# Optimization experiments

Hardware: AMD Instinct MI355X
Metric: run time of the kernel (lower is better)

## Reference

```python
import jax, jax.numpy as jnp
import numpy as np


def _dnn(a, b):
    # tf.math.divide_no_nan
    safe = jnp.where(b == 0, 1.0, b)
    return jnp.where(b == 0, 0.0, a / safe)


def _safe_sqrt(x):
    # _sqrt: 0 where x == 0 (grad-safe)
    p = x > 0
    return jnp.where(p, jnp.sqrt(jnp.where(p, x, 1.0)), 0.0)


def _agg4(v):
    # mean/var/skew/kurt over last axis, using the sample skew/kurt formulas
    # from _skewness2/_kurtosis2 in the source.
    n = float(v.shape[-1])
    m = jnp.mean(v, -1)
    c = v - m[..., None]
    var = jnp.mean(c ** 2, -1)
    std = _safe_sqrt(var)
    skew = n / ((n - 1.0) * (n - 2.0)) * jnp.sum(_dnn(c, std[..., None]) ** 3, -1)
    k4 = jnp.sum(c ** 4, -1)
    k22 = jnp.sum(c ** 2, -1) ** 2
    alpha = n * (n + 1.0) * (n - 1.0) / (n - 2.0) / (n - 3.0)
    kurt = alpha * _dnn(k4, k22) - 3.0 * (n - 1.0) ** 2 / (n - 2.0) / (n - 3.0)
    return m, var, skew, kurt


def _forward(x):
    B, T, F = x.shape
    nT = float(T)

    mean = jnp.mean(x, 1)                        # [B,F]
    xc = x - mean[:, None, :]                    # x_sub_means
    var = jnp.mean(xc ** 2, 1)                   # population variance
    std = _safe_sqrt(var)
    # diff: conv kernel [0,1,-1] VALID -> d[t] = x[t+1] - x[t+2], len T-2
    xd = x[:, 1:-1, :] - x[:, 2:, :]
    xd_abs = jnp.abs(xd)

    scal = [mean,
            jnp.min(x, 1), jnp.max(x, 1),
            _safe_sqrt(jnp.mean(x ** 2, 1)),      # rms
            var, std]
    # skewness / kurtosis over time (exact formulas from source)
    skew = nT / ((nT - 1.0) * (nT - 2.0)) * jnp.sum(_dnn(xc, std[:, None, :]) ** 3, 1)
    k4 = jnp.sum(xc ** 4, 1)
    k22 = jnp.sum(xc ** 2, 1) ** 2
    alpha = nT * (nT + 1.0) * (nT - 1.0) / (nT - 2.0) / (nT - 3.0)
    kurt = alpha * _dnn(k4, k22) - 3.0 * (nT - 1.0) ** 2 / (nT - 2.0) / (nT - 3.0)
    scal += [skew, kurt,
             jnp.mean(xd, 1), jnp.sum(xd, 1), jnp.mean(xd_abs, 1),  # change stats
             jnp.sum(x ** 2, 1),                  # abs_energy
             jnp.max(jnp.abs(x), 1),              # abs_max
             jnp.sum(xd_abs, 1),                  # abs_sum_of_changes
             _safe_sqrt(jnp.sum(xd ** 2, 1))]     # cid_ce

    # quantiles (sorted) and time-based quantiles
    xs = jnp.sort(x, axis=1)
    q_idx = [round(p * T) for p in (0.25, 0.5, 0.75)]
    q = xs[:, q_idx, :]                           # [B,3,F]
    tb_idx = [min(round(p * T), T - 1) for p in (0.0, 0.25, 0.5, 0.75, 1.0)]
    tb = x[:, tb_idx, :]                          # [B,5,F]

    def count_above(sgn):
        # count_above_zero: T - count_nonzero(sign - 1) == #(sign == 1)
        return jnp.sum(sgn == 1, 1).astype(x.dtype)

    def crossings(sgn):
        return jnp.sum(sgn[:, 1:, :] != sgn[:, :-1, :], 1).astype(x.dtype)

    s_x = jnp.sign(x)
    s_c = jnp.sign(xc)
    s_tb = [jnp.sign(x - tb[:, i:i + 1, :]) for i in range(5)]
    s_q = [jnp.sign(x - q[:, i:i + 1, :]) for i in range(3)]

    scal += [count_above(s_x), count_above(s_c)] + [count_above(s) for s in s_tb]
    scal += [crossings(s_x), crossings(s_c)]
    scal += [crossings(s) for s in s_q]
    scal += [crossings(s) for s in s_tb]

    # FFT features
    fx = jnp.fft.rfft(x, axis=1)                  # [B, T//2+1, F]
    amp = jnp.transpose(jnp.abs(fx), (0, 2, 1))   # [B,F,nf]
    ang = jnp.transpose(jnp.angle(fx), (0, 2, 1))
    ratio = _dnn(amp, jnp.sum(amp, -1, keepdims=True))
    am, av, ask, aku = _agg4(amp)
    rm, rv, rsk, rku = _agg4(ratio)
    scal += [amp[:, :, 0], am, av, ask, aku, rm, rv, rsk, rku]

    # autocorrelation (lags 1..9), matching _autocorrelation:
    # ac[l] = sum_t xc[t]*xc[t+l] / (T - l) / variance
    lags = list(range(1, 10))
    ac = jnp.stack([_dnn(jnp.sum(xc[:, :T - l, :] * xc[:, l:, :], 1) / (nT - l), var)
                    for l in lags], axis=-1)      # [B,F,9]
    acm, acv, acs, ack = _agg4(ac)
    ac_rmax = _dnn(ac, jnp.max(ac, -1, keepdims=True))
    scal += [acm, acv, acs, ack]

    out = jnp.concatenate(
        [jnp.stack(scal, -1),                     # [B,F,45]
         jnp.transpose(q, (0, 2, 1)),             # [B,F,3]
         jnp.transpose(tb, (0, 2, 1)),            # [B,F,5]
         amp, ang, ratio,                         # [B,F,1025] each
         ac, ac_rmax], axis=-1)                   # [B,F,9] each
    return out                                    # [B,F,3146]


def setup_inputs() -> dict:
    key = jax.random.key(0)
    x = jax.random.normal(key, (512, 2048, 16), dtype=jnp.float32)
    return {"x": x}


def reference(x):
    return _forward(x)
```

## Files before the change

### kernel.cpp

```cpp
#include <hip/hip_runtime.h>
#include <math.h>

#define T_LEN 2048
#define NF    16
#define NTH   256
#define NOUT  3146
#define PI_F  3.14159265358979323846f

__device__ __forceinline__ float wred_sum(float v) {
  v += __shfl_down(v, 32); v += __shfl_down(v, 16); v += __shfl_down(v, 8);
  v += __shfl_down(v, 4);  v += __shfl_down(v, 2);  v += __shfl_down(v, 1);
  return v;
}
__device__ __forceinline__ float wred_min(float v) {
  v = fminf(v, __shfl_down(v, 32)); v = fminf(v, __shfl_down(v, 16)); v = fminf(v, __shfl_down(v, 8));
  v = fminf(v, __shfl_down(v, 4));  v = fminf(v, __shfl_down(v, 2));  v = fminf(v, __shfl_down(v, 1));
  return v;
}
__device__ __forceinline__ float wred_max(float v) {
  v = fmaxf(v, __shfl_down(v, 32)); v = fmaxf(v, __shfl_down(v, 16)); v = fmaxf(v, __shfl_down(v, 8));
  v = fmaxf(v, __shfl_down(v, 4));  v = fmaxf(v, __shfl_down(v, 2));  v = fmaxf(v, __shfl_down(v, 1));
  return v;
}

template<int N>
__device__ __forceinline__ void block_sum_n(float (&v)[N], float* redw, float* res, int tid) {
  const int wave = tid >> 6;
#pragma unroll
  for (int j = 0; j < N; j++) {
    float s = wred_sum(v[j]);
    if ((tid & 63) == 0) redw[j * 4 + wave] = s;
  }
  __syncthreads();
  if (tid < N) res[tid] = redw[tid * 4] + redw[tid * 4 + 1] + redw[tid * 4 + 2] + redw[tid * 4 + 3];
  __syncthreads();
}

__device__ __forceinline__ void agg4_9(const float* v, float* om, float* ov, float* os, float* ok) {
  const float fn = 9.0f;
  float s = 0.f;
#pragma unroll
  for (int i = 0; i < 9; i++) s += v[i];
  float m = s / fn;
  float c2 = 0.f, c3 = 0.f, c4 = 0.f;
#pragma unroll
  for (int i = 0; i < 9; i++) {
    float c = v[i] - m; float cc = c * c;
    c2 += cc; c3 += cc * c; c4 += cc * cc;
  }
  float var = c2 / fn;
  float sd = (var > 0.f) ? sqrtf(var) : 0.f;
  float sk = (sd > 0.f) ? fn / ((fn - 1.f) * (fn - 2.f)) * (c3 / (sd * sd * sd)) : 0.f;
  float k22 = c2 * c2;
  float al = fn * (fn + 1.f) * (fn - 1.f) / ((fn - 2.f) * (fn - 3.f));
  float ku = ((k22 > 0.f) ? al * c4 / k22 : 0.f)
             - 3.f * (fn - 1.f) * (fn - 1.f) / ((fn - 2.f) * (fn - 3.f));
  *om = m; *ov = var; *os = sk; *ok = ku;
}

__device__ __forceinline__ float ord2f(unsigned int u) {
  unsigned int v = (u & 0x80000000u) ? (u ^ 0x80000000u) : ~u;
  return __uint_as_float(v);
}
__device__ __forceinline__ unsigned int f2ord(float v) {
  unsigned int u = __float_as_uint(v);
  return (u & 0x80000000u) ? ~u : (u | 0x80000000u);
}

__device__ __forceinline__ float fast_atan2f(float y, float x) {
  float ay = fabsf(y), ax = fabsf(x);
  float mx = fmaxf(ax, ay), mn = fminf(ax, ay);
  if (mx == 0.f) return 0.f;
  float t = __fdividef(mn, mx);
  float s = t * t;
  float p = fmaf(s, fmaf(s, fmaf(s, fmaf(s, 0.0208351f, -0.0851330f), 0.1801410f), -0.3302995f), 0.9998660f);
  float r = t * p;
  if (ay > ax) r = 1.57079632679f - r;
  if (x < 0.f) r = PI_F - r;
  return (y < 0.f) ? -r : r;
}

__global__ __launch_bounds__(NTH)
void ts_feat_kernel(const float* __restrict__ x, float* __restrict__ out, int gpx) {
  __shared__ __align__(16) float a[T_LEN];
  __shared__ __align__(16) unsigned int U[2048];
  __shared__ float redw[96];
  __shared__ float res[24];
  __shared__ unsigned int selres[8];

  float* zr = a;
  float* zi = a + 1024;
  float* Tc = (float*)U;
  float* Ts = (float*)U + 1024;

  const int tid = threadIdx.x;
  const int lane = tid & 63;
  const int wave = tid >> 6;
  int b, f;
  {
    int i = blockIdx.x;
    if (gpx > 0) { int xc = i & 7; int slot = i >> 3; b = xc * gpx + (slot >> 4); f = slot & 15; }
    else { b = i >> 4; f = i & 15; }
  }
  const float* xp = x + ((size_t)b * T_LEN) * NF + f;
  float* op = out + (size_t)(b * NF + f) * NOUT;
  const float fT = (float)T_LEN;

#pragma unroll
  for (int k = 0; k < 5; k++) U[tid + k * NTH] = 0u;

  unsigned int key[8];
  float s1 = 0.f, s2 = 0.f, s3 = 0.f, s4 = 0.f, mn = 3.4e38f, mx = -3.4e38f;
#pragma unroll
  for (int k = 0; k < 8; k++) {
    int t = tid + k * NTH;
    float v = xp[(size_t)t * NF];
    a[t] = v;
    key[k] = f2ord(v);
    float v2 = v * v;
    s1 += v; s2 += v2; s3 += v2 * v; s4 += v2 * v2;
    mn = fminf(mn, v); mx = fmaxf(mx, v);
  }
  s1 = wred_sum(s1); s2 = wred_sum(s2); s3 = wred_sum(s3); s4 = wred_sum(s4);
  mn = wred_min(mn); mx = wred_max(mx);
  if (lane == 0) {
    redw[wave] = s1; redw[4 + wave] = s2; redw[8 + wave] = s3; redw[12 + wave] = s4;
    redw[16 + wave] = mn; redw[20 + wave] = mx;
  }
  __syncthreads();

  const int woff = wave << 8;
#pragma unroll
  for (int k = 0; k < 8; k++) atomicAdd(&U[woff + (key[k] >> 24)], 1u);
  if (tid == 0) {
    res[0] = redw[0] + redw[1] + redw[2] + redw[3];
    res[1] = redw[4] + redw[5] + redw[6] + redw[7];
    res[2] = redw[8] + redw[9] + redw[10] + redw[11];
    res[3] = redw[12] + redw[13] + redw[14] + redw[15];
    res[4] = fminf(fminf(redw[16], redw[17]), fminf(redw[18], redw[19]));
    res[5] = fmaxf(fmaxf(redw[20], redw[21]), fmaxf(redw[22], redw[23]));
  }
  __syncthreads();

  float S1 = res[0], S2v = res[1], S3v = res[2], S4v = res[3], MN = res[4], MX = res[5];
  float mean = S1 / fT;
  float maxabs = fmaxf(-MN, MX);
  float rms = sqrtf(fmaxf(S2v / fT, 0.f));

  if (tid < 64) {
    const int l = tid;
    unsigned int b0 = U[4*l]   + U[256+4*l]   + U[512+4*l]   + U[768+4*l];
    unsigned int b1 = U[4*l+1] + U[256+4*l+1] + U[512+4*l+1] + U[768+4*l+1];
    unsigned int b2 = U[4*l+2] + U[256+4*l+2] + U[512+4*l+2] + U[768+4*l+2];
    unsigned int b3 = U[4*l+3] + U[256+4*l+3] + U[512+4*l+3] + U[768+4*l+3];
    unsigned int t0 = b0, t1 = t0 + b1, t2 = t1 + b2, t3 = t2 + b3;
    unsigned int tot = t3;
#pragma unroll
    for (int off = 1; off < 64; off <<= 1) {
      unsigned int n = __shfl_up(tot, off);
      if (l >= off) tot += n;
    }
    unsigned int base0 = tot - t3;
    U[1024+4*l] = base0+t0; U[1024+4*l+1] = base0+t1; U[1024+4*l+2] = base0+t2; U[1024+4*l+3] = base0+t3;
  }

  float v13[13];
  {
    const int base = tid * 8;
    const float4* a4 = (const float4*)a;
    float4 w0 = a4[tid*2], w1 = a4[tid*2+1];
    int i2 = (base + 11 < T_LEN) ? tid*2+2 : 0;
    int i3 = (base + 15 < T_LEN) ? tid*2+3 : 0;
    float4 w2 = a4[i2], w3 = a4[i3];
    bool ok2 = (base + 11 < T_LEN), ok3 = (base + 15 < T_LEN);
    float r[17];
    r[0]=w0.x; r[1]=w0.y; r[2]=w0.z; r[3]=w0.w;
    r[4]=w1.x; r[5]=w1.y; r[6]=w1.z; r[7]=w1.w;
    r[8]  = ok2 ? w2.x : mean; r[9]  = ok2 ? w2.y : mean; r[10] = ok2 ? w2.z : mean; r[11] = ok2 ? w2.w : mean;
    r[12] = ok3 ? w3.x : mean; r[13] = ok3 ? w3.y : mean; r[14] = ok3 ? w3.z : mean; r[15] = ok3 ? w3.w : mean;
    r[16] = (base + 16 < T_LEN) ? a[base + 16] : mean;
#pragma unroll
    for (int j = 0; j < 13; j++) v13[j] = 0.f;
#pragma unroll
    for (int j = 0; j < 8; j++) {
      if (base + j < T_LEN - 2) {
        float d = r[j+1] - r[j+2];
        v13[0] += d; v13[1] += fabsf(d); v13[2] += d * d;
      }
    }
#pragma unroll
    for (int l = 1; l <= 9; l++) {
#pragma unroll
      for (int j = 0; j < 8; j++) {
        v13[2 + l] += (r[j] - mean) * (r[j + l] - mean);
      }
    }
#pragma unroll
    for (int j = 0; j < 8; j++) {
      float c = r[j] - mean;
      v13[12] += c * c;
    }
  }
  __syncthreads();

  unsigned int prefix[3];
  unsigned int rank[3];
  {
    unsigned int incl = U[1024 + tid];
    unsigned int excl = (tid == 0) ? 0u : U[1024 + tid - 1];
    const unsigned int rks[3] = {512u, 1024u, 1536u};
#pragma unroll
    for (int j = 0; j < 3; j++)
      if (excl <= rks[j] && rks[j] < incl) { selres[2*j] = (unsigned)tid; selres[2*j+1] = rks[j] - excl; }
    U[tid] = 0u; U[tid + 256] = 0u; U[tid + 512] = 0u;
  }

  block_sum_n<13>(v13, redw, res, tid);
  float SD = res[0], SAD = res[1], SDD = res[2];
  float C2w = res[12];
  float var = C2w / fT;
  float sd = (var > 0.f) ? sqrtf(var) : 0.f;
  float C3 = S3v - 3.f*mean*S2v + 2.f*fT*mean*mean*mean;
  float mm = mean * mean;
  float C4 = S4v - 4.f*mean*S3v + 6.f*mm*S2v - 3.f*fT*mm*mm;
  float skw = (sd > 0.f) ? (fT / ((fT - 1.f) * (fT - 2.f))) * (C3 / (sd * sd * sd)) : 0.f;
  float k22 = C2w * C2w;
  float alphaT = fT * (fT + 1.f) * (fT - 1.f) / ((fT - 2.f) * (fT - 3.f));
  float kurt = ((k22 > 0.f) ? alphaT * C4 / k22 : 0.f)
               - 3.f * (fT - 1.f) * (fT - 1.f) / ((fT - 2.f) * (fT - 3.f));
  float ac[9], acm, acv, acs, ack, acmax;
  {
    float invvar = (var != 0.f) ? 1.f / var : 0.f;
#pragma unroll
    for (int l = 1; l <= 9; l++) ac[l-1] = res[2 + l] / (fT - (float)l) * invvar;
    agg4_9(ac, &acm, &acv, &acs, &ack);
    acmax = ac[0];
#pragma unroll
    for (int l = 1; l < 9; l++) acmax = fmaxf(acmax, ac[l]);
  }
#pragma unroll
  for (int j = 0; j < 3; j++) { prefix[j] = selres[2*j] << 24; rank[j] = selres[2*j+1]; }

  for (int rnd = 1; rnd < 4; rnd++) {
    const int shift = 24 - 8 * rnd;
#pragma unroll
    for (int k = 0; k < 8; k++) {
      unsigned int u = key[k];
      unsigned int hi = u >> (shift + 8);
#pragma unroll
      for (int j = 0; j < 3; j++) {
        if (hi == (prefix[j] >> (shift + 8)))
          atomicAdd(&U[j * 256 + ((u >> shift) & 255u)], 1u);
      }
    }
    __syncthreads();
    if (tid < 192) {
      int w = tid >> 6, l = tid & 63;
      unsigned int* h = U + w * 256;
      unsigned int b0 = h[4*l], b1 = h[4*l+1], b2 = h[4*l+2], b3 = h[4*l+3];
      unsigned int t0 = b0, t1 = t0+b1, t2 = t1+b2, t3 = t2+b3;
      unsigned int tot = t3;
#pragma unroll
      for (int off = 1; off < 64; off <<= 1) {
        unsigned int n = __shfl_up(tot, off);
        if (l >= off) tot += n;
      }
      unsigned int base0 = tot - t3;
      unsigned int* c = U + 768 + w * 256;
      c[4*l] = base0+t0; c[4*l+1] = base0+t1; c[4*l+2] = base0+t2; c[4*l+3] = base0+t3;
    }
    __syncthreads();
    if (tid < 192) {
      int j = tid >> 6, l = tid & 63;
#pragma unroll
      for (int i = 0; i < 4; i++) {
        int bk = 4 * l + i;
        unsigned int incl = U[768 + j * 256 + bk];
        unsigned int excl = (bk == 0) ? 0u : U[768 + j * 256 + bk - 1];
        if (excl <= rank[j] && rank[j] < incl) { selres[2*j] = (unsigned)bk; selres[2*j+1] = rank[j] - excl; }
      }
    } else if (rnd < 3) {
      int z0 = (tid - 192) * 12;
#pragma unroll
      for (int k = 0; k < 12; k++) U[z0 + k] = 0u;
    }
    __syncthreads();
#pragma unroll
    for (int j = 0; j < 3; j++) { prefix[j] |= selres[2*j] << shift; rank[j] = selres[2*j+1]; }
  }
  float q0 = ord2f(prefix[0]), q1 = ord2f(prefix[1]), q2 = ord2f(prefix[2]);
  float tb0 = a[0], tb1 = a[512], tb2 = a[1024], tb3 = a[1536], tb4 = a[2047];

  {
    const unsigned int kt0 = f2ord(0.f), kt1 = f2ord(mean), kt2 = prefix[0], kt3 = prefix[1], kt4 = prefix[2];
    const unsigned int kt5 = f2ord(tb0), kt6 = f2ord(tb1), kt7 = f2ord(tb2), kt8 = f2ord(tb3), kt9 = f2ord(tb4);
    int cnt0=0,cnt1=0,cnt2=0,cnt3=0,cnt4=0,cnt5=0,cnt6=0,cnt7=0,cnt8=0,cnt9=0;
    int crs0=0,crs1=0,crs2=0,crs3=0,crs4=0,crs5=0,crs6=0,crs7=0,crs8=0,crs9=0;
#pragma unroll
    for (int k = 0; k < 8; k++) {
      unsigned int kv = key[k];
#define BAL(J, KT)                                                        \
      { unsigned long long mp = __ballot(kv > (KT));                      \
        unsigned long long mz = __ballot(kv == (KT));                     \
        cnt##J += (int)__popcll(mp);                                      \
        unsigned long long df = ((mp ^ (mp >> 1)) | (mz ^ (mz >> 1)))     \
                                & 0x7fffffffffffffffull;                  \
        crs##J += (int)__popcll(df); }
      BAL(0, kt0) BAL(1, kt1) BAL(2, kt2) BAL(3, kt3) BAL(4, kt4)
      BAL(5, kt5) BAL(6, kt6) BAL(7, kt7) BAL(8, kt8) BAL(9, kt9)
#undef BAL
    }
    if (tid < 64) {
      unsigned long long pk = 0ull;
      if (tid < 31) {
        float a0 = a[64*tid + 63], a1 = a[64*tid + 64];
#define SEAMB(J, TH)                                                      \
        { bool g0 = a0 > (TH), g1 = a1 > (TH);                            \
          bool e0 = a0 == (TH), e1 = a1 == (TH);                          \
          if ((g0 != g1) || (e0 != e1)) pk |= (1ull << (6*(J))); }
        SEAMB(0, 0.f) SEAMB(1, mean) SEAMB(2, q0) SEAMB(3, q1) SEAMB(4, q2)
        SEAMB(5, tb0) SEAMB(6, tb1) SEAMB(7, tb2) SEAMB(8, tb3) SEAMB(9, tb4)
#undef SEAMB
      }
      pk += __shfl_down(pk, 32); pk += __shfl_down(pk, 16); pk += __shfl_down(pk, 8);
      pk += __shfl_down(pk, 4);  pk += __shfl_down(pk, 2);  pk += __shfl_down(pk, 1);
      if (tid == 0) {
#pragma unroll
        for (int j = 0; j < 10; j++) redw[80 + j] = (float)((unsigned int)((pk >> (6*j)) & 63ull));
      }
    }
    if (lane == 0) {
      int w20 = wave * 20;
      redw[w20+0]=(float)cnt0; redw[w20+1]=(float)cnt1; redw[w20+2]=(float)cnt2;
      redw[w20+3]=(float)cnt3; redw[w20+4]=(float)cnt4; redw[w20+5]=(float)cnt5;
      redw[w20+6]=(float)cnt6; redw[w20+7]=(float)cnt7; redw[w20+8]=(float)cnt8;
      redw[w20+9]=(float)cnt9;
      redw[w20+10]=(float)crs0; redw[w20+11]=(float)crs1; redw[w20+12]=(float)crs2;
      redw[w20+13]=(float)crs3; redw[w20+14]=(float)crs4; redw[w20+15]=(float)crs5;
      redw[w20+16]=(float)crs6; redw[w20+17]=(float)crs7; redw[w20+18]=(float)crs8;
      redw[w20+19]=(float)crs9;
    }
  }

  {
    float cs, sn;
    __sincosf(-PI_F * (float)tid * (1.f / 256.f), &sn, &cs);
    const float cd = 0.9999952938095762f;
    const float sd_ = -0.0030679567629659761f;
#pragma unroll
    for (int j = 0; j < 4; j++) {
      int k = 4 * tid + j;
      int xk = k ^ (k >> 5);
      Tc[xk] = cs; Ts[xk] = sn;
      float ncs = cs * cd - sn * sd_;
      float nsn = sn * cd + cs * sd_;
      cs = ncs; sn = nsn;
    }
  }

  float2 rz0, rz1, rz2, rz3;
  {
    const float2* a2 = (const float2*)a;
    rz0 = a2[tid]; rz1 = a2[tid + 256]; rz2 = a2[tid + 512]; rz3 = a2[tid + 768];
  }
  __syncthreads();

  if (tid < 20) {
    float s = redw[tid] + redw[20 + tid] + redw[40 + tid] + redw[60 + tid];
    if (tid >= 10) s += redw[80 + (tid - 10)];
    res[4 + tid] = s;
  }
  {
#define SCAT(K, Z)                                                     \
    { int p = tid + (K) * 256;                                         \
      int rl = (int)(__brev((unsigned)(p & 31)) >> 27);                \
      int c = p >> 5;                                                  \
      int idx = rl * 32 + (c ^ rl);                                    \
      zr[idx] = (Z).x; zi[idx] = (Z).y; }
    SCAT(0, rz0) SCAT(1, rz1) SCAT(2, rz2) SCAT(3, rz3)
#undef SCAT
  }
  __syncthreads();
  float gr[4], gi[4];
#pragma unroll
  for (int k = 0; k < 4; k++) {
    int m = tid + k * 256;
    int h = m >> 5, l = m & 31;
    int rl5 = (int)(__brev((unsigned)l) >> 27);
    int idx = h * 32 + (rl5 ^ h);
    gr[k] = zr[idx]; gi[k] = zi[idx];
  }
  __syncthreads();
#pragma unroll
  for (int k = 0; k < 4; k++) { int m = tid + k * 256; zr[m] = gr[k]; zi[m] = gi[k]; }
  __syncthreads();

  {
    float4 R = ((const float4*)zr)[tid];
    float4 I = ((const float4*)zi)[tid];
    float u0r = R.x + R.y, u0i = I.x + I.y;
    float u1r = R.x - R.y, u1i = I.x - I.y;
    float u2r = R.z + R.w, u2i = I.z + I.w;
    float u3r = R.z - R.w, u3i = I.z - I.w;
    float4 Ro, Io;
    Ro.x = u0r + u2r; Io.x = u0i + u2i;
    Ro.z = u0r - u2r; Io.z = u0i - u2i;
    Ro.y = u1r + u3i; Io.y = u1i - u3r;
    Ro.w = u1r - u3i; Io.w = u1i + u3r;
    ((float4*)zr)[tid] = Ro; ((float4*)zi)[tid] = Io;
  }
#pragma unroll
  for (int p = 1; p < 5; p++) {
    const int hf = 1 << (2 * p);
    __syncthreads();
    const int qq = tid & (hf - 1);
    const int i0 = ((tid >> (2 * p)) << (2 * p + 2)) | qq;
    const int i1 = i0 + hf, i2 = i0 + 2 * hf, i3 = i0 + 3 * hf;
    const int t1 = qq << (10 - 2 * p);
    const int t2 = qq << (9 - 2 * p);
    const int t3 = t2 + 512;
    const int x1 = t1 ^ (t1 >> 5), x2 = t2 ^ (t2 >> 5), x3 = t3 ^ (t3 >> 5);
    float cA = Tc[x1], sA = Ts[x1];
    float cB = Tc[x2], sB = Ts[x2];
    float cC = Tc[x3], sC = Ts[x3];
    float r0 = zr[i0], m0 = zi[i0], r1 = zr[i1], m1 = zi[i1];
    float r2 = zr[i2], m2 = zi[i2], r3 = zr[i3], m3 = zi[i3];
    float a1r = cA*r1 - sA*m1, a1i = cA*m1 + sA*r1;
    float a3r = cA*r3 - sA*m3, a3i = cA*m3 + sA*r3;
    float u0r = r0 + a1r, u0i = m0 + a1i;
    float u1r = r0 - a1r, u1i = m0 - a1i;
    float u2r = r2 + a3r, u2i = m2 + a3i;
    float u3r = r2 - a3r, u3i = m2 - a3i;
    float b2r = cB*u2r - sB*u2i, b2i = cB*u2i + sB*u2r;
    float b3r = cC*u3r - sC*u3i, b3i = cC*u3i + sC*u3r;
    zr[i0] = u0r + b2r; zi[i0] = u0i + b2i;
    zr[i2] = u0r - b2r; zi[i2] = u0i - b2i;
    zr[i1] = u1r + b3r; zi[i1] = u1i + b3i;
    zr[i3] = u1r - b3r; zi[i3] = u1i - b3i;
  }
  __syncthreads();

  float ampv[4], angv[4];
  float v4[4] = {0.f, 0.f, 0.f, 0.f};
#pragma unroll
  for (int k = 0; k < 4; k++) {
    int kk = tid + k * NTH;
    int nk = (1024 - kk) & 1023;
    float z1r = zr[kk], z1i = zi[kk];
    float z2r = zr[nk], z2i = zi[nk];
    float Er = 0.5f * (z1r + z2r), Ei = 0.5f * (z1i - z2i);
    float Or = 0.5f * (z1i + z2i), Oi = -0.5f * (z1r - z2r);
    int xk = kk ^ (kk >> 5);
    float cs = Tc[xk], sn = Ts[xk];
    float Xr = Er + cs * Or - sn * Oi;
    float Xi = Ei + cs * Oi + sn * Or;
    float amp = sqrtf(Xr * Xr + Xi * Xi);
    ampv[k] = amp;
    angv[k] = fast_atan2f(Xi, Xr);
    float a2p = amp * amp;
    v4[0] += amp; v4[1] += a2p; v4[2] += a2p * amp; v4[3] += a2p * a2p;
  }
  float amp4 = 0.f, ang4 = 0.f;
  if (tid == 0) {
    float Xr = zr[0] - zi[0];
    amp4 = fabsf(Xr);
    ang4 = (Xr < 0.f) ? PI_F : 0.f;
    float a2p = amp4 * amp4;
    v4[0] += amp4; v4[1] += a2p; v4[2] += a2p * amp4; v4[3] += a2p * a2p;
  }
  block_sum_n<4>(v4, redw, res, tid);
  float S = res[0], M2 = res[1], M3 = res[2], M4 = res[3];
  const float fn = 1025.f;
  float am = S / fn;
  float A2 = M2 - fn * am * am;
  float A3 = M3 - 3.f * am * M2 + 2.f * fn * am * am * am;
  float am2 = am * am;
  float A4 = M4 - 4.f * am * M3 + 6.f * am2 * M2 - 3.f * fn * am2 * am2;
  float av = A2 / fn;
  float asd = (av > 0.f) ? sqrtf(av) : 0.f;
  float ask = (asd > 0.f) ? fn / ((fn - 1.f) * (fn - 2.f)) * (A3 / (asd * asd * asd)) : 0.f;
  float ak22 = A2 * A2;
  float aal = fn * (fn + 1.f) * (fn - 1.f) / ((fn - 2.f) * (fn - 3.f));
  float aku = ((ak22 > 0.f) ? aal * A4 / ak22 : 0.f)
              - 3.f * (fn - 1.f) * (fn - 1.f) / ((fn - 2.f) * (fn - 3.f));
  float invS = (S != 0.f) ? 1.f / S : 0.f;
  float rm = am * invS;
  float rv = av * invS * invS;

#pragma unroll
  for (int k = 0; k < 4; k++) {
    int kk = tid + k * NTH;
    op[53 + kk]   = ampv[k];
    op[1078 + kk] = angv[k];
    op[2103 + kk] = ampv[k] * invS;
  }
  if (tid < 9) {
    float acj;
    switch (tid) {
      case 0: acj = ac[0]; break; case 1: acj = ac[1]; break; case 2: acj = ac[2]; break;
      case 3: acj = ac[3]; break; case 4: acj = ac[4]; break; case 5: acj = ac[5]; break;
      case 6: acj = ac[6]; break; case 7: acj = ac[7]; break; default: acj = ac[8]; break;
    }
    op[3128 + tid] = acj;
    op[3137 + tid] = (acmax != 0.f) ? acj / acmax : 0.f;
  }
  if (tid == 0) {
    op[53 + 1024] = amp4; op[1078 + 1024] = ang4; op[2103 + 1024] = amp4 * invS;
    op[0] = mean; op[1] = MN; op[2] = MX; op[3] = rms; op[4] = var; op[5] = sd;
    op[6] = skw; op[7] = kurt;
    op[8] = SD / (fT - 2.f); op[9] = SD; op[10] = SAD / (fT - 2.f);
    op[11] = S2v; op[12] = maxabs; op[13] = SAD;
    op[14] = (SDD > 0.f) ? sqrtf(SDD) : 0.f;
    op[15] = res[4]; op[16] = res[5];
    op[17] = res[9]; op[18] = res[10]; op[19] = res[11]; op[20] = res[12]; op[21] = res[13];
    op[22] = res[14]; op[23] = res[15];
    op[24] = res[16]; op[25] = res[17]; op[26] = res[18];
    op[27] = res[19]; op[28] = res[20]; op[29] = res[21]; op[30] = res[22]; op[31] = res[23];
    op[32] = ampv[0];
    op[33] = am; op[34] = av; op[35] = ask; op[36] = aku;
    op[37] = rm; op[38] = rv; op[39] = ask; op[40] = aku;
    op[41] = acm; op[42] = acv; op[43] = acs; op[44] = ack;
    op[45] = q0; op[46] = q1; op[47] = q2;
    op[48] = tb0; op[49] = tb1; op[50] = tb2; op[51] = tb3; op[52] = tb4;
  }
}

extern "C" void kernel_launch(void* const* d_in, const int* in_sizes, int n_in,
                              void* d_out, int out_size, void* d_ws, size_t ws_size,
                              hipStream_t stream) {
  const float* x = (const float*)d_in[0];
  float* out = (float*)d_out;
  const int total = in_sizes[0];
  const int B = total / (T_LEN * NF);
  const int nblocks = B * NF;
  const int gpx = (B % 8 == 0) ? (B / 8) : 0;
  ts_feat_kernel<<<nblocks, NTH, 0, stream>>>(x, out, gpx);
}
```

Before: 204.2 us.

## Restructure quantile radix select to 11+7+7+7 bits and cheapen atan2 polynomial

The radix select for the three quantiles now uses an 11-bit first pass into a single shared 2048-bin histogram, followed by three 7-bit refinement rounds instead of four 8-bit rounds. Per-thread register prefix sums replace the per-wave histograms and the extra scan/search barriers, and bins are cleared inline. The 13-value block reduction is fused with the first scan's barrier, and centered values are precomputed once for the autocorrelation sums. The atan2 polynomial is cut from degree 9 to degree 5, which lowers accuracy of the phase output and could exceed the tolerance.

```diff
diff --git a/kernel.cpp b/kernel.cpp
--- a/kernel.cpp
+++ b/kernel.cpp
@@ -73,7 +73,7 @@
   if (mx == 0.f) return 0.f;
   float t = __fdividef(mn, mx);
   float s = t * t;
-  float p = fmaf(s, fmaf(s, fmaf(s, fmaf(s, 0.0208351f, -0.0851330f), 0.1801410f), -0.3302995f), 0.9998660f);
+  float p = fmaf(s, fmaf(s, 0.079331f, -0.288679f), 0.995354f);
   float r = t * p;
   if (ay > ax) r = 1.57079632679f - r;
   if (x < 0.f) r = PI_F - r;
@@ -87,6 +87,7 @@
   __shared__ float redw[96];
   __shared__ float res[24];
   __shared__ unsigned int selres[8];
+  __shared__ unsigned int wtot[4];
 
   float* zr = a;
   float* zi = a + 1024;
@@ -107,7 +108,7 @@
   const float fT = (float)T_LEN;
 
 #pragma unroll
-  for (int k = 0; k < 5; k++) U[tid + k * NTH] = 0u;
+  for (int k = 0; k < 8; k++) U[tid + k * NTH] = 0u;
 
   unsigned int key[8];
   float s1 = 0.f, s2 = 0.f, s3 = 0.f, s4 = 0.f, mn = 3.4e38f, mx = -3.4e38f;
@@ -129,9 +130,8 @@
   }
   __syncthreads();
 
-  const int woff = wave << 8;
-#pragma unroll
-  for (int k = 0; k < 8; k++) atomicAdd(&U[woff + (key[k] >> 24)], 1u);
+#pragma unroll
+  for (int k = 0; k < 8; k++) atomicAdd(&U[key[k] >> 21], 1u);
   if (tid == 0) {
     res[0] = redw[0] + redw[1] + redw[2] + redw[3];
     res[1] = redw[4] + redw[5] + redw[6] + redw[7];
@@ -147,22 +147,21 @@
   float maxabs = fmaxf(-MN, MX);
   float rms = sqrtf(fmaxf(S2v / fT, 0.f));
 
-  if (tid < 64) {
-    const int l = tid;
-    unsigned int b0 = U[4*l]   + U[256+4*l]   + U[512+4*l]   + U[768+4*l];
-    unsigned int b1 = U[4*l+1] + U[256+4*l+1] + U[512+4*l+1] + U[768+4*l+1];
-    unsigned int b2 = U[4*l+2] + U[256+4*l+2] + U[512+4*l+2] + U[768+4*l+2];
-    unsigned int b3 = U[4*l+3] + U[256+4*l+3] + U[512+4*l+3] + U[768+4*l+3];
-    unsigned int t0 = b0, t1 = t0 + b1, t2 = t1 + b2, t3 = t2 + b3;
-    unsigned int tot = t3;
-#pragma unroll
-    for (int off = 1; off < 64; off <<= 1) {
-      unsigned int n = __shfl_up(tot, off);
-      if (l >= off) tot += n;
-    }
-    unsigned int base0 = tot - t3;
-    U[1024+4*l] = base0+t0; U[1024+4*l+1] = base0+t1; U[1024+4*l+2] = base0+t2; U[1024+4*l+3] = base0+t3;
-  }
+  uint4 h0 = ((const uint4*)U)[2 * tid];
+  uint4 h1 = ((const uint4*)U)[2 * tid + 1];
+  if (tid < 48) {
+    uint4 z; z.x = 0u; z.y = 0u; z.z = 0u; z.w = 0u;
+    ((uint4*)U)[2 * tid] = z; ((uint4*)U)[2 * tid + 1] = z;
+  }
+  unsigned c1 = h0.x, c2 = c1 + h0.y, c3 = c2 + h0.z, c4 = c3 + h0.w;
+  unsigned c5 = c4 + h1.x, c6 = c5 + h1.y, c7 = c6 + h1.z, tot = c7 + h1.w;
+  unsigned sc = tot;
+#pragma unroll
+  for (int off = 1; off < 64; off <<= 1) {
+    unsigned n = __shfl_up(sc, off);
+    if (lane >= off) sc += n;
+  }
+  if (lane == 63) wtot[wave] = sc;
 
   float v13[13];
   {
@@ -179,6 +178,9 @@
     r[8]  = ok2 ? w2.x : mean; r[9]  = ok2 ? w2.y : mean; r[10] = ok2 ? w2.z : mean; r[11] = ok2 ? w2.w : mean;
     r[12] = ok3 ? w3.x : mean; r[13] = ok3 ? w3.y : mean; r[14] = ok3 ? w3.z : mean; r[15] = ok3 ? w3.w : mean;
     r[16] = (base + 16 < T_LEN) ? a[base + 16] : mean;
+    float cw[17];
+#pragma unroll
+    for (int j = 0; j < 17; j++) cw[j] = r[j] - mean;
 #pragma unroll
     for (int j = 0; j < 13; j++) v13[j] = 0.f;
 #pragma unroll
@@ -192,30 +194,48 @@
     for (int l = 1; l <= 9; l++) {
 #pragma unroll
       for (int j = 0; j < 8; j++) {
-        v13[2 + l] += (r[j] - mean) * (r[j + l] - mean);
-      }
-    }
-#pragma unroll
-    for (int j = 0; j < 8; j++) {
-      float c = r[j] - mean;
-      v13[12] += c * c;
-    }
-  }
-  __syncthreads();
-
-  unsigned int prefix[3];
-  unsigned int rank[3];
-  {
-    unsigned int incl = U[1024 + tid];
-    unsigned int excl = (tid == 0) ? 0u : U[1024 + tid - 1];
-    const unsigned int rks[3] = {512u, 1024u, 1536u};
-#pragma unroll
-    for (int j = 0; j < 3; j++)
-      if (excl <= rks[j] && rks[j] < incl) { selres[2*j] = (unsigned)tid; selres[2*j+1] = rks[j] - excl; }
-    U[tid] = 0u; U[tid + 256] = 0u; U[tid + 512] = 0u;
-  }
-
-  block_sum_n<13>(v13, redw, res, tid);
+        v13[2 + l] += cw[j] * cw[j + l];
+      }
+    }
+#pragma unroll
+    for (int j = 0; j < 8; j++) v13[12] += cw[j] * cw[j];
+  }
+  {
+#pragma unroll
+    for (int j = 0; j < 13; j++) {
+      float s = wred_sum(v13[j]);
+      if (lane == 0) redw[j * 4 + wave] = s;
+    }
+  }
+  __syncthreads();
+
+  if (tid < 13) res[tid] = redw[tid*4] + redw[tid*4+1] + redw[tid*4+2] + redw[tid*4+3];
+  {
+    unsigned base0 = 0;
+    if (wave > 0) base0 += wtot[0];
+    if (wave > 1) base0 += wtot[1];
+    if (wave > 2) base0 += wtot[2];
+    unsigned excl = base0 + sc - tot;
+#pragma unroll
+    for (int j = 0; j < 3; j++) {
+      const unsigned rj = 512u * (unsigned)(j + 1);
+      if (rj >= excl && rj < excl + tot) {
+        unsigned r = rj - excl;
+        unsigned bin, resid;
+        if      (r < c1) { bin = 0u; resid = r; }
+        else if (r < c2) { bin = 1u; resid = r - c1; }
+        else if (r < c3) { bin = 2u; resid = r - c2; }
+        else if (r < c4) { bin = 3u; resid = r - c3; }
+        else if (r < c5) { bin = 4u; resid = r - c4; }
+        else if (r < c6) { bin = 5u; resid = r - c5; }
+        else if (r < c7) { bin = 6u; resid = r - c6; }
+        else             { bin = 7u; resid = r - c7; }
+        selres[2*j] = 8u * (unsigned)tid + bin; selres[2*j+1] = resid;
+      }
+    }
+  }
+  __syncthreads();
+
   float SD = res[0], SAD = res[1], SDD = res[2];
   float C2w = res[12];
   float var = C2w / fT;
@@ -238,51 +258,42 @@
 #pragma unroll
     for (int l = 1; l < 9; l++) acmax = fmaxf(acmax, ac[l]);
   }
-#pragma unroll
-  for (int j = 0; j < 3; j++) { prefix[j] = selres[2*j] << 24; rank[j] = selres[2*j+1]; }
-
-  for (int rnd = 1; rnd < 4; rnd++) {
-    const int shift = 24 - 8 * rnd;
+  unsigned int prefix[3], rank[3];
+#pragma unroll
+  for (int j = 0; j < 3; j++) { prefix[j] = selres[2*j] << 21; rank[j] = selres[2*j+1]; }
+
+#pragma unroll
+  for (int rnd = 0; rnd < 3; rnd++) {
+    const int shift = 14 - 7 * rnd;
+    const int pshift = shift + 7;
 #pragma unroll
     for (int k = 0; k < 8; k++) {
-      unsigned int u = key[k];
-      unsigned int hi = u >> (shift + 8);
+      unsigned u = key[k];
+      unsigned hi = u >> pshift;
 #pragma unroll
       for (int j = 0; j < 3; j++) {
-        if (hi == (prefix[j] >> (shift + 8)))
-          atomicAdd(&U[j * 256 + ((u >> shift) & 255u)], 1u);
+        if (hi == (prefix[j] >> pshift))
+          atomicAdd(&U[j * 128 + ((u >> shift) & 127u)], 1u);
       }
     }
     __syncthreads();
     if (tid < 192) {
-      int w = tid >> 6, l = tid & 63;
-      unsigned int* h = U + w * 256;
-      unsigned int b0 = h[4*l], b1 = h[4*l+1], b2 = h[4*l+2], b3 = h[4*l+3];
-      unsigned int t0 = b0, t1 = t0+b1, t2 = t1+b2, t3 = t2+b3;
-      unsigned int tot = t3;
+      int j = wave, l = lane;
+      unsigned h0v = U[j*128 + 2*l], h1v = U[j*128 + 2*l + 1];
+      U[j*128 + 2*l] = 0u; U[j*128 + 2*l + 1] = 0u;
+      unsigned tt = h0v + h1v;
+      unsigned sc2 = tt;
 #pragma unroll
       for (int off = 1; off < 64; off <<= 1) {
-        unsigned int n = __shfl_up(tot, off);
-        if (l >= off) tot += n;
-      }
-      unsigned int base0 = tot - t3;
-      unsigned int* c = U + 768 + w * 256;
-      c[4*l] = base0+t0; c[4*l+1] = base0+t1; c[4*l+2] = base0+t2; c[4*l+3] = base0+t3;
-    }
-    __syncthreads();
-    if (tid < 192) {
-      int j = tid >> 6, l = tid & 63;
-#pragma unroll
-      for (int i = 0; i < 4; i++) {
-        int bk = 4 * l + i;
-        unsigned int incl = U[768 + j * 256 + bk];
-        unsigned int excl = (bk == 0) ? 0u : U[768 + j * 256 + bk - 1];
-        if (excl <= rank[j] && rank[j] < incl) { selres[2*j] = (unsigned)bk; selres[2*j+1] = rank[j] - excl; }
-      }
-    } else if (rnd < 3) {
-      int z0 = (tid - 192) * 12;
-#pragma unroll
-      for (int k = 0; k < 12; k++) U[z0 + k] = 0u;
+        unsigned n = __shfl_up(sc2, off);
+        if (l >= off) sc2 += n;
+      }
+      unsigned ex = sc2 - tt;
+      unsigned rj = rank[j];
+      if (rj >= ex && rj < ex + tt) {
+        if (rj < ex + h0v) { selres[2*j] = 2u*l;     selres[2*j+1] = rj - ex; }
+        else               { selres[2*j] = 2u*l + 1u; selres[2*j+1] = rj - ex - h0v; }
+      }
     }
     __syncthreads();
 #pragma unroll
```

Measured after the change: 213.7 us. +4.6%, slower.
